# Optimization experiments

Measured on AMD Instinct MI355X. Metric: run time of the kernel, lower is better.

Reference implementation:

```python
import jax, jax.numpy as jnp
import numpy as np
import math

H = 12  # num heads
EPS = 1e-5


def layer_norm(x, g, b):
    xf = x.astype(jnp.float32)
    mu = jnp.mean(xf, axis=-1, keepdims=True)
    var = jnp.var(xf, axis=-1, keepdims=True)
    return ((xf - mu) * jax.lax.rsqrt(var + EPS) * g + b).astype(x.dtype)


def setup_inputs() -> dict:
    key = jax.random.key(0)
    ks = jax.random.split(key, 8)
    C, M = 768, 3072
    s = 0.02
    inp = {
        "x": jax.random.normal(ks[0], (128, 197, C), dtype=jnp.float32),
        # linear weights stored as [in, out] (y = x @ W + b)
        "Wq": jax.random.normal(ks[1], (C, C), dtype=jnp.float32) * s,
        "bq": jnp.zeros((C,), jnp.float32),
        "Wk": jax.random.normal(ks[2], (C, C), dtype=jnp.float32) * s,
        "bk": jnp.zeros((C,), jnp.float32),
        "Wv": jax.random.normal(ks[3], (C, C), dtype=jnp.float32) * s,
        "bv": jnp.zeros((C,), jnp.float32),
        "Wo": jax.random.normal(ks[4], (C, C), dtype=jnp.float32) * s,
        "bo": jnp.zeros((C,), jnp.float32),
        "W1": jax.random.normal(ks[5], (C, M), dtype=jnp.float32) * s,
        "b1": jnp.zeros((M,), jnp.float32),
        "W2": jax.random.normal(ks[6], (M, C), dtype=jnp.float32) * s,
        "b2": jnp.zeros((C,), jnp.float32),
        "g1": jnp.ones((C,), jnp.float32),
        "beta1": jnp.zeros((C,), jnp.float32),
        "g2": jnp.ones((C,), jnp.float32),
        "beta2": jnp.zeros((C,), jnp.float32),
    }
    return inp


def attention(xn, Wq, bq, Wk, bk, Wv, bv, Wo, bo):
    N, L, C = xn.shape
    Cqk = C // H
    q = (xn @ Wq + bq).reshape(N, L, H, Cqk)
    k = (xn @ Wk + bk).reshape(N, L, H, Cqk)
    v = (xn @ Wv + bv).reshape(N, L, H, Cqk)
    scale = 1.0 / math.sqrt(Cqk)
    aff = jnp.einsum('nqhc,nkhc->nqkh', q * scale, k)  # [N, Lq, Lk, H]
    aff = jax.nn.softmax(aff, axis=-2)                  # softmax over key axis
    mix = jnp.einsum('nqlh,nlhc->nqhc', aff, v)
    return mix.reshape(N, L, C) @ Wo + bo


def reference(x, Wq, bq, Wk, bk, Wv, bv, Wo, bo, W1, b1, W2, b2, g1, beta1, g2, beta2):
    x = x + attention(layer_norm(x, g1, beta1), Wq, bq, Wk, bk, Wv, bv, Wo, bo)
    h = layer_norm(x, g2, beta2) @ W1 + b1
    h = h * jax.nn.sigmoid(1.702 * h)  # QuickGELU
    return x + h @ W2 + b2
```

## Files before the change

kernel.cpp:

```cpp
#include <hip/hip_runtime.h>
#include <hip/hip_bf16.h>

typedef __bf16 bf16_t;
typedef __bf16 bf16x8 __attribute__((ext_vector_type(8)));
typedef float f32x4 __attribute__((ext_vector_type(4)));

#define T_TOK 25216
#define C_DIM 768
#define NH 12
#define LSEQ 197

__device__ __forceinline__ void gload_lds16(const bf16_t* g, bf16_t* l) {
  __builtin_amdgcn_global_load_lds(
      (const __attribute__((address_space(1))) unsigned int*)g,
      (__attribute__((address_space(3))) unsigned int*)l, 16, 0, 0);
}

template <int N>
__device__ __forceinline__ void vm_wait() {
  asm volatile("s_waitcnt vmcnt(%0)" ::"n"(N) : "memory");
}
__device__ __forceinline__ void block_bar() {
  __builtin_amdgcn_sched_barrier(0);
  asm volatile("" ::: "memory");
  __builtin_amdgcn_s_barrier();
  __builtin_amdgcn_sched_barrier(0);
}

__global__ void wtrans_k(const float* __restrict__ W, bf16_t* __restrict__ Wt,
                         int K, int N) {
  __shared__ float tile[32][33];
  const int tx = threadIdx.x, ty = threadIdx.y;
  const int bx = blockIdx.x, by = blockIdx.y;
#pragma unroll
  for (int i = ty; i < 32; i += 8)
    tile[i][tx] = W[(long)(by * 32 + i) * N + bx * 32 + tx];
  __syncthreads();
#pragma unroll
  for (int i = ty; i < 32; i += 8)
    Wt[(long)(bx * 32 + i) * K + by * 32 + tx] = (bf16_t)tile[tx][i];
}

__global__ void cat3_k(const float* __restrict__ a, const float* __restrict__ b,
                       const float* __restrict__ c, float* __restrict__ o) {
  int i = blockIdx.x * 256 + threadIdx.x;
  if (i < 2304) o[i] = i < 768 ? a[i] : (i < 1536 ? b[i - 768] : c[i - 1536]);
}

__global__ __launch_bounds__(256) void ln_k(const float* __restrict__ x,
                                            const float* __restrict__ g,
                                            const float* __restrict__ b,
                                            bf16_t* __restrict__ o) {
  const int lane = threadIdx.x & 63;
  const long row = (long)blockIdx.x * 4 + (threadIdx.x >> 6);
  const float* xr = x + row * C_DIM;
  float4 v[3];
  float s = 0.f, sq = 0.f;
#pragma unroll
  for (int i = 0; i < 3; ++i) {
    v[i] = *(const float4*)&xr[i * 256 + lane * 4];
    s += v[i].x + v[i].y + v[i].z + v[i].w;
    sq += v[i].x * v[i].x + v[i].y * v[i].y + v[i].z * v[i].z + v[i].w * v[i].w;
  }
#pragma unroll
  for (int off = 32; off; off >>= 1) {
    s += __shfl_xor(s, off);
    sq += __shfl_xor(sq, off);
  }
  const float mu = s * (1.f / 768.f);
  const float rstd = rsqrtf(sq * (1.f / 768.f) - mu * mu + 1e-5f);
  bf16_t* orow = o + row * C_DIM;
#pragma unroll
  for (int i = 0; i < 3; ++i) {
    const int c = i * 256 + lane * 4;
    const float4 gg = *(const float4*)&g[c];
    const float4 bb = *(const float4*)&b[c];
    bf16_t t4[4];
    t4[0] = (bf16_t)((v[i].x - mu) * rstd * gg.x + bb.x);
    t4[1] = (bf16_t)((v[i].y - mu) * rstd * gg.y + bb.y);
    t4[2] = (bf16_t)((v[i].z - mu) * rstd * gg.z + bb.z);
    t4[3] = (bf16_t)((v[i].w - mu) * rstd * gg.w + bb.w);
    __builtin_memcpy(&orow[c], t4, 8);
  }
}

template <int EPI, int BM, int BN>
__global__ __launch_bounds__(256) void gemm_bt(
    const bf16_t* __restrict__ A, const bf16_t* __restrict__ Bt,
    const float* __restrict__ bias, const float* __restrict__ res,
    void* __restrict__ outp, int K, int N) {
  constexpr int MACC = BM / 32;
  constexpr int NACC = BN / 32;
  constexpr int ACW = BM / 32;
  constexpr int BCW = BN / 32;
  constexpr int NLOADS = ACW + BCW;
  __shared__ __align__(16) bf16_t lA[2][BM * 64];
  __shared__ __align__(16) bf16_t lB[2][BN * 64];
  const int tid = threadIdx.x;
  const int wave = tid >> 6, lane = tid & 63;
  const int fr = lane & 15, fq = lane >> 4;

  const int gx = gridDim.x;
  const int nwg = gridDim.x * gridDim.y;
  int bid = blockIdx.y * gx + blockIdx.x;
  {
    const int q = nwg >> 3, r = nwg & 7;
    const int xcd = bid & 7, idx = bid >> 3;
    bid = (xcd < r ? xcd * (q + 1) : r * (q + 1) + (xcd - r) * q) + idx;
  }
  const int bx = bid % gx, by = bid / gx;

  const long rowBase = (long)by * BM;
  const long colBase = (long)bx * BN;
  const int wr = (wave >> 1) * (BM / 2), wc = (wave & 1) * (BN / 2);

  f32x4 acc[MACC][NACC];
#pragma unroll
  for (int m = 0; m < MACC; ++m)
#pragma unroll
    for (int n = 0; n < NACC; ++n) acc[m][n] = (f32x4){0.f, 0.f, 0.f, 0.f};

  const int srow = lane >> 3;
  const int scol = (((lane & 7) ^ srow)) * 8;

  const bf16_t* aP[ACW];
  const bf16_t* bP[BCW];
#pragma unroll
  for (int c = 0; c < ACW; ++c)
    aP[c] = A + (rowBase + 8 * (wave * ACW + c) + srow) * (long)K + scol;
#pragma unroll
  for (int c = 0; c < BCW; ++c)
    bP[c] = Bt + (colBase + 8 * (wave * BCW + c) + srow) * (long)K + scol;

  auto stage0 = [&](int koff) {
#pragma unroll
    for (int c = 0; c < ACW; ++c)
      gload_lds16(aP[c] + koff, &lA[0][(wave * ACW + c) * 512]);
#pragma unroll
    for (int c = 0; c < BCW; ++c)
      gload_lds16(bP[c] + koff, &lB[0][(wave * BCW + c) * 512]);
  };
  auto stage1 = [&](int koff) {
#pragma unroll
    for (int c = 0; c < ACW; ++c)
      gload_lds16(aP[c] + koff, &lA[1][(wave * ACW + c) * 512]);
#pragma unroll
    for (int c = 0; c < BCW; ++c)
      gload_lds16(bP[c] + koff, &lB[1][(wave * BCW + c) * 512]);
  };
  auto compute0 = [&]() {
#pragma unroll
    for (int kf = 0; kf < 2; ++kf) {
      bf16x8 af[MACC], bfr[NACC];
#pragma unroll
      for (int m = 0; m < MACC; ++m) {
        const int row = wr + m * 16 + fr;
        af[m] =
            *(const bf16x8*)&lA[0][row * 64 + (((kf * 4 + fq) ^ (fr & 7)) * 8)];
      }
#pragma unroll
      for (int n = 0; n < NACC; ++n) {
        const int row = wc + n * 16 + fr;
        bfr[n] =
            *(const bf16x8*)&lB[0][row * 64 + (((kf * 4 + fq) ^ (fr & 7)) * 8)];
      }
#pragma unroll
      for (int m = 0; m < MACC; ++m)
#pragma unroll
        for (int n = 0; n < NACC; ++n)
          acc[m][n] = __builtin_amdgcn_mfma_f32_16x16x32_bf16(af[m], bfr[n],
                                                              acc[m][n], 0, 0, 0);
    }
  };
  auto compute1 = [&]() {
#pragma unroll
    for (int kf = 0; kf < 2; ++kf) {
      bf16x8 af[MACC], bfr[NACC];
#pragma unroll
      for (int m = 0; m < MACC; ++m) {
        const int row = wr + m * 16 + fr;
        af[m] =
            *(const bf16x8*)&lA[1][row * 64 + (((kf * 4 + fq) ^ (fr & 7)) * 8)];
      }
#pragma unroll
      for (int n = 0; n < NACC; ++n) {
        const int row = wc + n * 16 + fr;
        bfr[n] =
            *(const bf16x8*)&lB[1][row * 64 + (((kf * 4 + fq) ^ (fr & 7)) * 8)];
      }
#pragma unroll
      for (int m = 0; m < MACC; ++m)
#pragma unroll
        for (int n = 0; n < NACC; ++n)
          acc[m][n] = __builtin_amdgcn_mfma_f32_16x16x32_bf16(af[m], bfr[n],
                                                              acc[m][n], 0, 0, 0);
    }
  };

  const int kT = K >> 6;
  stage0(0);
  int kt = 0;
  for (; kt + 2 < kT; kt += 2) {
    stage1((kt + 1) * 64);
    vm_wait<NLOADS>();
    block_bar();
    compute0();
    block_bar();
    stage0((kt + 2) * 64);
    vm_wait<NLOADS>();
    block_bar();
    compute1();
    block_bar();
  }
  stage1((kt + 1) * 64);
  vm_wait<NLOADS>();
  block_bar();
  compute0();
  vm_wait<0>();
  block_bar();
  compute1();

#pragma unroll
  for (int m = 0; m < MACC; ++m) {
    const long row0 = rowBase + wr + m * 16 + fq * 4;
#pragma unroll
    for (int n = 0; n < NACC; ++n) {
      const long col = colBase + wc + n * 16 + fr;
      const float bb = bias[col];
#pragma unroll
      for (int r = 0; r < 4; ++r) {
        const long idx = (row0 + r) * N + col;
        float v = acc[m][n][r] + bb;
        if (EPI == 0) {
          ((bf16_t*)outp)[idx] = (bf16_t)v;
        } else if (EPI == 1) {
          ((float*)outp)[idx] = v + res[idx];
        } else {
          v = v / (1.f + __expf(-1.702f * v));
          ((bf16_t*)outp)[idx] = (bf16_t)v;
        }
      }
    }
  }
}

__global__ __launch_bounds__(256) void attn_k(const bf16_t* __restrict__ qkv,
                                              bf16_t* __restrict__ mix) {
  constexpr int KR = 72;
  constexpr int VR = 232;
  __shared__ __align__(16) bf16_t smem[208 * KR + 64 * VR + 64 * VR];
  bf16_t* lK = smem;
  bf16_t* lVt = smem + 208 * KR;
  bf16_t* lP = lVt + 64 * VR;

  const int tid = threadIdx.x;
  const int wave = tid >> 6, lane = tid & 63;
  const int fr = lane & 15, fq = lane >> 4;
  const int nh = blockIdx.x;
  const int n = nh / NH, h = nh % NH;
  const long t0 = (long)n * LSEQ;
  const long qs = 2304;

  {
    int4 z = {0, 0, 0, 0};
    int4* p = (int4*)smem;
    const int tot = (208 * KR + 2 * 64 * VR) * 2 / 16;
    for (int i = tid; i < tot; i += 256) p[i] = z;
  }
  __syncthreads();

  for (int it = tid; it < 197 * 8; it += 256) {
    int r = it >> 3, cg = it & 7;
    int4 v = *(const int4*)(qkv + (t0 + r) * qs + 768 + h * 64 + cg * 8);
    *(int4*)&lK[r * KR + cg * 8] = v;
  }
  for (int it = tid; it < 197 * 8; it += 256) {
    int r = it >> 3, cg = it & 7;
    int4 v = *(const int4*)(qkv + (t0 + r) * qs + 1536 + h * 64 + cg * 8);
    const bf16_t* pv = (const bf16_t*)&v;
#pragma unroll
    for (int j = 0; j < 8; ++j) lVt[(cg * 8 + j) * VR + r] = pv[j];
  }
  __syncthreads();

  bf16_t* lPw = lP + wave * 16 * VR;

  for (int fi = 0; fi < 4; ++fi) {
    const int f = wave + fi * 4;
    if (f >= 13) break;
    const int qrow = f * 16 + fr;
    const long tq = t0 + (qrow < LSEQ ? qrow : LSEQ - 1);
    const bf16_t* qp = qkv + tq * qs + h * 64;
    bf16x8 a0 = *(const bf16x8*)(qp + fq * 8);
    bf16x8 a1 = *(const bf16x8*)(qp + 32 + fq * 8);

    f32x4 s[13];
#pragma unroll
    for (int j = 0; j < 13; ++j) s[j] = (f32x4){0.f, 0.f, 0.f, 0.f};
#pragma unroll
    for (int j = 0; j < 13; ++j) {
      bf16x8 b0 = *(const bf16x8*)&lK[(j * 16 + fr) * KR + fq * 8];
      s[j] = __builtin_amdgcn_mfma_f32_16x16x32_bf16(a0, b0, s[j], 0, 0, 0);
      bf16x8 b1 = *(const bf16x8*)&lK[(j * 16 + fr) * KR + 32 + fq * 8];
      s[j] = __builtin_amdgcn_mfma_f32_16x16x32_bf16(a1, b1, s[j], 0, 0, 0);
    }
    float mx[4] = {-3e38f, -3e38f, -3e38f, -3e38f};
#pragma unroll
    for (int j = 0; j < 13; ++j) {
      const bool valid = (j * 16 + fr) < LSEQ;
#pragma unroll
      for (int r = 0; r < 4; ++r) {
        float v = s[j][r] * 0.125f;
        v = valid ? v : -3e38f;
        s[j][r] = v;
        mx[r] = fmaxf(mx[r], v);
      }
    }
#pragma unroll
    for (int r = 0; r < 4; ++r) {
      mx[r] = fmaxf(mx[r], __shfl_xor(mx[r], 1));
      mx[r] = fmaxf(mx[r], __shfl_xor(mx[r], 2));
      mx[r] = fmaxf(mx[r], __shfl_xor(mx[r], 4));
      mx[r] = fmaxf(mx[r], __shfl_xor(mx[r], 8));
    }
    float sm[4] = {0.f, 0.f, 0.f, 0.f};
#pragma unroll
    for (int j = 0; j < 13; ++j)
#pragma unroll
      for (int r = 0; r < 4; ++r) {
        float e = __expf(s[j][r] - mx[r]);
        s[j][r] = e;
        sm[r] += e;
      }
#pragma unroll
    for (int r = 0; r < 4; ++r) {
      sm[r] += __shfl_xor(sm[r], 1);
      sm[r] += __shfl_xor(sm[r], 2);
      sm[r] += __shfl_xor(sm[r], 4);
      sm[r] += __shfl_xor(sm[r], 8);
      sm[r] = 1.f / sm[r];
    }
#pragma unroll
    for (int j = 0; j < 13; ++j)
#pragma unroll
      for (int r = 0; r < 4; ++r)
        lPw[(fq * 4 + r) * VR + j * 16 + fr] = (bf16_t)(s[j][r] * sm[r]);
    asm volatile("s_waitcnt lgkmcnt(0)" ::: "memory");

    f32x4 o4[4];
#pragma unroll
    for (int c = 0; c < 4; ++c) o4[c] = (f32x4){0.f, 0.f, 0.f, 0.f};
#pragma unroll
    for (int kc = 0; kc < 7; ++kc) {
      bf16x8 pa = *(const bf16x8*)&lPw[fr * VR + kc * 32 + fq * 8];
#pragma unroll
      for (int c = 0; c < 4; ++c) {
        bf16x8 bv = *(const bf16x8*)&lVt[(c * 16 + fr) * VR + kc * 32 + fq * 8];
        o4[c] = __builtin_amdgcn_mfma_f32_16x16x32_bf16(pa, bv, o4[c], 0, 0, 0);
      }
    }
#pragma unroll
    for (int c = 0; c < 4; ++c)
#pragma unroll
      for (int r = 0; r < 4; ++r) {
        const int q = f * 16 + fq * 4 + r;
        if (q < LSEQ)
          mix[(t0 + q) * C_DIM + h * 64 + c * 16 + fr] = (bf16_t)o4[c][r];
      }
  }
}

extern "C" void kernel_launch(void* const* d_in, const int* in_sizes, int n_in,
                              void* d_out, int out_size, void* d_ws,
                              size_t ws_size, hipStream_t stream) {
  const float* x = (const float*)d_in[0];
  const float* Wq = (const float*)d_in[1];
  const float* bq = (const float*)d_in[2];
  const float* Wk = (const float*)d_in[3];
  const float* bk = (const float*)d_in[4];
  const float* Wv = (const float*)d_in[5];
  const float* bv = (const float*)d_in[6];
  const float* Wo = (const float*)d_in[7];
  const float* bo = (const float*)d_in[8];
  const float* W1 = (const float*)d_in[9];
  const float* b1 = (const float*)d_in[10];
  const float* W2 = (const float*)d_in[11];
  const float* b2 = (const float*)d_in[12];
  const float* g1 = (const float*)d_in[13];
  const float* be1 = (const float*)d_in[14];
  const float* g2 = (const float*)d_in[15];
  const float* be2 = (const float*)d_in[16];

  char* ws = (char*)d_ws;
  size_t off = 0;
  auto alloc = [&](size_t bytes) {
    char* p = ws + off;
    off += (bytes + 255) & ~(size_t)255;
    return p;
  };
  bf16_t* xn = (bf16_t*)alloc((size_t)T_TOK * 768 * 2);
  char* qm = alloc((size_t)T_TOK * 3072 * 2);
  bf16_t* qkv = (bf16_t*)qm;
  bf16_t* mixb = (bf16_t*)(qm + (size_t)T_TOK * 2304 * 2);
  bf16_t* h = (bf16_t*)qm;
  bf16_t* Wqkvt = (bf16_t*)alloc((size_t)2304 * 768 * 2);
  bf16_t* Wot = (bf16_t*)alloc((size_t)768 * 768 * 2);
  bf16_t* W1t = (bf16_t*)alloc((size_t)3072 * 768 * 2);
  bf16_t* W2t = (bf16_t*)alloc((size_t)768 * 3072 * 2);
  float* bqkv = (float*)alloc(2304 * 4);
  float* x2 = (float*)d_out;

  dim3 tb(32, 8);
  wtrans_k<<<dim3(24, 24), tb, 0, stream>>>(Wq, Wqkvt, 768, 768);
  wtrans_k<<<dim3(24, 24), tb, 0, stream>>>(Wk, Wqkvt + 768 * 768, 768, 768);
  wtrans_k<<<dim3(24, 24), tb, 0, stream>>>(Wv, Wqkvt + 2 * 768 * 768, 768, 768);
  wtrans_k<<<dim3(24, 24), tb, 0, stream>>>(Wo, Wot, 768, 768);
  wtrans_k<<<dim3(96, 24), tb, 0, stream>>>(W1, W1t, 768, 3072);
  wtrans_k<<<dim3(24, 96), tb, 0, stream>>>(W2, W2t, 3072, 768);
  cat3_k<<<9, 256, 0, stream>>>(bq, bk, bv, bqkv);

  ln_k<<<T_TOK / 4, 256, 0, stream>>>(x, g1, be1, xn);
  gemm_bt<0, 128, 128><<<dim3(2304 / 128, T_TOK / 128), 256, 0, stream>>>(
      xn, Wqkvt, bqkv, nullptr, qkv, 768, 2304);
  attn_k<<<128 * NH, 256, 0, stream>>>(qkv, mixb);
  gemm_bt<1, 128, 128><<<dim3(768 / 128, T_TOK / 128), 256, 0, stream>>>(
      mixb, Wot, bo, x, x2, 768, 768);
  ln_k<<<T_TOK / 4, 256, 0, stream>>>(x2, g2, be2, xn);
  gemm_bt<2, 128, 128><<<dim3(3072 / 128, T_TOK / 128), 256, 0, stream>>>(
      xn, W1t, b1, nullptr, h, 768, 3072);
  gemm_bt<1, 128, 128><<<dim3(768 / 128, T_TOK / 128), 256, 0, stream>>>(
      h, W2t, b2, x2, (float*)d_out, 3072, 768);
}
```

Before: 718.8 us.

## Switch GEMM inner loop to 32x32x16 MFMA and merge weight transposes

The GEMM kernel now computes each wave's 64x64 sub-tile with 2x2 32x32x16 bf16 MFMAs instead of 4x4 16x16x32 MFMAs. This changes the LDS fragment addressing and the epilogue's output row/column mapping. Larger MFMA tiles mean fewer LDS fragment reads per FLOP and fewer instruction issues. The four 768x768 weight transposes are merged into one launch over a z-dimension to cut launch overhead. The epilogue now stores with a 32-lane column pattern, which may change how well global stores coalesce.

```diff
diff --git a/kernel.cpp b/kernel.cpp
--- a/kernel.cpp
+++ b/kernel.cpp
@@ -4,6 +4,7 @@
 typedef __bf16 bf16_t;
 typedef __bf16 bf16x8 __attribute__((ext_vector_type(8)));
 typedef float f32x4 __attribute__((ext_vector_type(4)));
+typedef float f32x16 __attribute__((ext_vector_type(16)));
 
 #define T_TOK 25216
 #define C_DIM 768
@@ -25,6 +26,25 @@
   asm volatile("" ::: "memory");
   __builtin_amdgcn_s_barrier();
   __builtin_amdgcn_sched_barrier(0);
+}
+
+__global__ void wtrans4_k(const float* __restrict__ Wq,
+                          const float* __restrict__ Wk,
+                          const float* __restrict__ Wv,
+                          const float* __restrict__ Wo,
+                          bf16_t* __restrict__ Wqkvt, bf16_t* __restrict__ Wot) {
+  __shared__ float tile[32][33];
+  const int tx = threadIdx.x, ty = threadIdx.y;
+  const int bx = blockIdx.x, by = blockIdx.y, z = blockIdx.z;
+  const float* W = z == 0 ? Wq : (z == 1 ? Wk : (z == 2 ? Wv : Wo));
+  bf16_t* Wt = z == 3 ? Wot : Wqkvt + (size_t)z * 768 * 768;
+#pragma unroll
+  for (int i = ty; i < 32; i += 8)
+    tile[i][tx] = W[(long)(by * 32 + i) * 768 + bx * 32 + tx];
+  __syncthreads();
+#pragma unroll
+  for (int i = ty; i < 32; i += 8)
+    Wt[(long)(bx * 32 + i) * 768 + by * 32 + tx] = (bf16_t)tile[tx][i];
 }
 
 __global__ void wtrans_k(const float* __restrict__ W, bf16_t* __restrict__ Wt,
@@ -89,8 +109,8 @@
     const bf16_t* __restrict__ A, const bf16_t* __restrict__ Bt,
     const float* __restrict__ bias, const float* __restrict__ res,
     void* __restrict__ outp, int K, int N) {
-  constexpr int MACC = BM / 32;
-  constexpr int NACC = BN / 32;
+  constexpr int MW = BM / 64;
+  constexpr int NW = BN / 64;
   constexpr int ACW = BM / 32;
   constexpr int BCW = BN / 32;
   constexpr int NLOADS = ACW + BCW;
@@ -98,7 +118,7 @@
   __shared__ __align__(16) bf16_t lB[2][BN * 64];
   const int tid = threadIdx.x;
   const int wave = tid >> 6, lane = tid & 63;
-  const int fr = lane & 15, fq = lane >> 4;
+  const int l31 = lane & 31, lh = lane >> 5;
 
   const int gx = gridDim.x;
   const int nwg = gridDim.x * gridDim.y;
@@ -114,11 +134,13 @@
   const long colBase = (long)bx * BN;
   const int wr = (wave >> 1) * (BM / 2), wc = (wave & 1) * (BN / 2);
 
-  f32x4 acc[MACC][NACC];
-#pragma unroll
-  for (int m = 0; m < MACC; ++m)
-#pragma unroll
-    for (int n = 0; n < NACC; ++n) acc[m][n] = (f32x4){0.f, 0.f, 0.f, 0.f};
+  f32x16 acc[MW][NW];
+#pragma unroll
+  for (int m = 0; m < MW; ++m)
+#pragma unroll
+    for (int n = 0; n < NW; ++n)
+#pragma unroll
+      for (int e = 0; e < 16; ++e) acc[m][n][e] = 0.f;
 
   const int srow = lane >> 3;
   const int scol = (((lane & 7) ^ srow)) * 8;
@@ -150,49 +172,39 @@
   };
   auto compute0 = [&]() {
 #pragma unroll
-    for (int kf = 0; kf < 2; ++kf) {
-      bf16x8 af[MACC], bfr[NACC];
-#pragma unroll
-      for (int m = 0; m < MACC; ++m) {
-        const int row = wr + m * 16 + fr;
-        af[m] =
-            *(const bf16x8*)&lA[0][row * 64 + (((kf * 4 + fq) ^ (fr & 7)) * 8)];
-      }
-#pragma unroll
-      for (int n = 0; n < NACC; ++n) {
-        const int row = wc + n * 16 + fr;
-        bfr[n] =
-            *(const bf16x8*)&lB[0][row * 64 + (((kf * 4 + fq) ^ (fr & 7)) * 8)];
-      }
-#pragma unroll
-      for (int m = 0; m < MACC; ++m)
-#pragma unroll
-        for (int n = 0; n < NACC; ++n)
-          acc[m][n] = __builtin_amdgcn_mfma_f32_16x16x32_bf16(af[m], bfr[n],
+    for (int ks = 0; ks < 4; ++ks) {
+      const int cs = ((ks * 2 + lh) ^ (l31 & 7)) * 8;
+      bf16x8 af[MW], bv[NW];
+#pragma unroll
+      for (int m = 0; m < MW; ++m)
+        af[m] = *(const bf16x8*)&lA[0][(wr + m * 32 + l31) * 64 + cs];
+#pragma unroll
+      for (int n = 0; n < NW; ++n)
+        bv[n] = *(const bf16x8*)&lB[0][(wc + n * 32 + l31) * 64 + cs];
+#pragma unroll
+      for (int m = 0; m < MW; ++m)
+#pragma unroll
+        for (int n = 0; n < NW; ++n)
+          acc[m][n] = __builtin_amdgcn_mfma_f32_32x32x16_bf16(af[m], bv[n],
                                                               acc[m][n], 0, 0, 0);
     }
   };
   auto compute1 = [&]() {
 #pragma unroll
-    for (int kf = 0; kf < 2; ++kf) {
-      bf16x8 af[MACC], bfr[NACC];
-#pragma unroll
-      for (int m = 0; m < MACC; ++m) {
-        const int row = wr + m * 16 + fr;
-        af[m] =
-            *(const bf16x8*)&lA[1][row * 64 + (((kf * 4 + fq) ^ (fr & 7)) * 8)];
-      }
-#pragma unroll
-      for (int n = 0; n < NACC; ++n) {
-        const int row = wc + n * 16 + fr;
-        bfr[n] =
-            *(const bf16x8*)&lB[1][row * 64 + (((kf * 4 + fq) ^ (fr & 7)) * 8)];
-      }
-#pragma unroll
-      for (int m = 0; m < MACC; ++m)
-#pragma unroll
-        for (int n = 0; n < NACC; ++n)
-          acc[m][n] = __builtin_amdgcn_mfma_f32_16x16x32_bf16(af[m], bfr[n],
+    for (int ks = 0; ks < 4; ++ks) {
+      const int cs = ((ks * 2 + lh) ^ (l31 & 7)) * 8;
+      bf16x8 af[MW], bv[NW];
+#pragma unroll
+      for (int m = 0; m < MW; ++m)
+        af[m] = *(const bf16x8*)&lA[1][(wr + m * 32 + l31) * 64 + cs];
+#pragma unroll
+      for (int n = 0; n < NW; ++n)
+        bv[n] = *(const bf16x8*)&lB[1][(wc + n * 32 + l31) * 64 + cs];
+#pragma unroll
+      for (int m = 0; m < MW; ++m)
+#pragma unroll
+        for (int n = 0; n < NW; ++n)
+          acc[m][n] = __builtin_amdgcn_mfma_f32_32x32x16_bf16(af[m], bv[n],
                                                               acc[m][n], 0, 0, 0);
     }
   };
@@ -221,23 +233,27 @@
   compute1();
 
 #pragma unroll
-  for (int m = 0; m < MACC; ++m) {
-    const long row0 = rowBase + wr + m * 16 + fq * 4;
-#pragma unroll
-    for (int n = 0; n < NACC; ++n) {
-      const long col = colBase + wc + n * 16 + fr;
+  for (int m = 0; m < MW; ++m) {
+    const long rowb = rowBase + wr + m * 32 + 4 * lh;
+#pragma unroll
+    for (int n = 0; n < NW; ++n) {
+      const long col = colBase + wc + n * 32 + l31;
       const float bb = bias[col];
 #pragma unroll
-      for (int r = 0; r < 4; ++r) {
-        const long idx = (row0 + r) * N + col;
-        float v = acc[m][n][r] + bb;
-        if (EPI == 0) {
-          ((bf16_t*)outp)[idx] = (bf16_t)v;
-        } else if (EPI == 1) {
-          ((float*)outp)[idx] = v + res[idx];
-        } else {
-          v = v / (1.f + __expf(-1.702f * v));
-          ((bf16_t*)outp)[idx] = (bf16_t)v;
+      for (int rg = 0; rg < 4; ++rg) {
+#pragma unroll
+        for (int rr = 0; rr < 4; ++rr) {
+          const long row = rowb + rr + 8 * rg;
+          const long idx = row * N + col;
+          float v = acc[m][n][rg * 4 + rr] + bb;
+          if (EPI == 0) {
+            ((bf16_t*)outp)[idx] = (bf16_t)v;
+          } else if (EPI == 1) {
+            ((float*)outp)[idx] = v + res[idx];
+          } else {
+            v = v / (1.f + __expf(-1.702f * v));
+            ((bf16_t*)outp)[idx] = (bf16_t)v;
+          }
         }
       }
     }
@@ -411,10 +427,7 @@
   float* x2 = (float*)d_out;
 
   dim3 tb(32, 8);
-  wtrans_k<<<dim3(24, 24), tb, 0, stream>>>(Wq, Wqkvt, 768, 768);
-  wtrans_k<<<dim3(24, 24), tb, 0, stream>>>(Wk, Wqkvt + 768 * 768, 768, 768);
-  wtrans_k<<<dim3(24, 24), tb, 0, stream>>>(Wv, Wqkvt + 2 * 768 * 768, 768, 768);
-  wtrans_k<<<dim3(24, 24), tb, 0, stream>>>(Wo, Wot, 768, 768);
+  wtrans4_k<<<dim3(24, 24, 4), tb, 0, stream>>>(Wq, Wk, Wv, Wo, Wqkvt, Wot);
   wtrans_k<<<dim3(96, 24), tb, 0, stream>>>(W1, W1t, 768, 3072);
   wtrans_k<<<dim3(24, 96), tb, 0, stream>>>(W2, W2t, 3072, 768);
   cat3_k<<<9, 256, 0, stream>>>(bq, bk, bv, bqkv);
```

Result: slower. 756.7 us (+5.3%).
